# Kernel optimization log

Measured on AMD Instinct MI355X. Metric: run time of the kernel, lower is better.

Reference implementation:

```python
import jax, jax.numpy as jnp
import numpy as np

DIM, D_INNER, D_STATE, DT_RANK, D_CONV = 1024, 2048, 16, 64, 4
BATCH, SEQ = 2, 1024

def setup_inputs() -> dict:
    key = jax.random.key(0)
    ks = jax.random.split(key, 9)
    s = 0.02
    A = jnp.tile(jnp.arange(1, D_STATE + 1, dtype=jnp.float32), (D_INNER, 1))
    return {
        "x": jax.random.normal(ks[0], (BATCH, SEQ, DIM), jnp.float32),
        "in_proj_w": jax.random.normal(ks[1], (DIM, 2 * D_INNER), jnp.float32) * s,
        "conv_w": jax.random.normal(ks[2], (D_INNER, 1, D_CONV), jnp.float32) * 0.2,
        "conv_b": jax.random.normal(ks[3], (D_INNER,), jnp.float32) * 0.1,
        "x_proj_w": jax.random.normal(ks[4], (D_INNER, DT_RANK + 2 * D_STATE), jnp.float32) * s,
        "dt_proj_w": jax.random.normal(ks[5], (DT_RANK, D_INNER), jnp.float32) * s,
        "dt_proj_b": jax.random.normal(ks[6], (D_INNER,), jnp.float32) * 0.1,
        "A_log": jnp.log(A),
        "D_param": jnp.ones((D_INNER,), jnp.float32),
        "out_proj_w": jax.random.normal(ks[7], (D_INNER, DIM), jnp.float32) * s,
    }

def _silu(v):
    return v * jax.nn.sigmoid(v)

def _ssm_forward(x, in_proj_w, conv_w, conv_b, x_proj_w, dt_proj_w, dt_proj_b, A_log, D_param, out_proj_w):
    b, l, _ = x.shape
    d_inner, d_conv = conv_w.shape[0], conv_w.shape[2]
    dt_rank, n = dt_proj_w.shape[0], A_log.shape[1]
    # input projection and split into conv branch / gate branch
    x_and_res = x @ in_proj_w                      # (b, l, 2*d_inner)
    xp, res = x_and_res[..., :d_inner], x_and_res[..., d_inner:]
    # causal depthwise conv (torch pads d_conv-1 both sides then slices [:l])
    h = jax.lax.conv_general_dilated(
        xp.transpose(0, 2, 1), conv_w,
        window_strides=(1,), padding=[(d_conv - 1, 0)],
        dimension_numbers=("NCH", "OIH", "NCH"),
        feature_group_count=d_inner,
    ) + conv_b[None, :, None]                      # (b, d_inner, l)
    h = _silu(h.transpose(0, 2, 1))                # (b, l, d_inner)
    # input-dependent SSM parameters
    A = -jnp.exp(A_log)                            # (d_inner, n)
    x_dbl = h @ x_proj_w                           # (b, l, dt_rank + 2n)
    dlt, Bm, Cm = (x_dbl[..., :dt_rank],
                   x_dbl[..., dt_rank:dt_rank + n],
                   x_dbl[..., dt_rank + n:])
    delta = jax.nn.softplus(dlt @ dt_proj_w + dt_proj_b)   # (b, l, d_inner)
    # discretization
    deltaA = jnp.exp(jnp.einsum("bld,dn->bldn", delta, A))             # (b,l,d,n)
    deltaB_u = (delta * h)[..., None] * Bm[:, :, None, :]              # (b,l,d,n)
    # sequential selective scan over time via lax.scan
    def step(state, t):
        dA_t, dBu_t, c_t = t
        state = dA_t * state + dBu_t               # (b, d, n)
        y_t = jnp.einsum("bdn,bn->bd", state, c_t)
        return state, y_t
    init = jnp.zeros((b, d_inner, n), h.dtype)
    _, ys = jax.lax.scan(step, init,
                         (deltaA.transpose(1, 0, 2, 3),
                          deltaB_u.transpose(1, 0, 2, 3),
                          Cm.transpose(1, 0, 2)))
    y = ys.transpose(1, 0, 2) + h * D_param        # (b, l, d_inner)
    y = y * _silu(res)
    return y @ out_proj_w                          # (b, l, dim)

def reference(x, in_proj_w, conv_w, conv_b, x_proj_w, dt_proj_w, dt_proj_b, A_log, D_param, out_proj_w):
    return _ssm_forward(x, in_proj_w, conv_w, conv_b, x_proj_w, dt_proj_w, dt_proj_b, A_log, D_param, out_proj_w)
```

## Files before the change

### kernel.cpp

```cpp
#include <hip/hip_runtime.h>
#include <hip/hip_bf16.h>

#define DIM     1024
#define DINNER  2048
#define NSTATE  16
#define DTRANK  64
#define DCONV   4
#define BATCH   2
#define SEQ     1024
#define BL      (BATCH*SEQ)
#define XDBLW   96
#define NCHUNK  32
#define TCHUNK  32
#define KSLICE  16
#define G4SK    4
#define LOG2E   1.44269504088896f
#define LN2     0.69314718055995f

typedef __attribute__((ext_vector_type(4))) float  f32x4;
typedef __attribute__((ext_vector_type(8))) short  bf16x8;
typedef unsigned short ushort_t;

__device__ __forceinline__ ushort_t f2bf(float f) {
    union { float f; unsigned int u; } v; v.f = f;
    unsigned int lsb = (v.u >> 16) & 1u;
    v.u += 0x7fffu + lsb;
    return (ushort_t)(v.u >> 16);
}
__device__ __forceinline__ float bf2f(ushort_t h) {
    union { unsigned u; float f; } v; v.u = ((unsigned)h) << 16; return v.f;
}
__device__ __forceinline__ float hexp2(float x) { return __builtin_amdgcn_exp2f(x); }
__device__ __forceinline__ float hlog2(float x) { return __builtin_amdgcn_logf(x); }
__device__ __forceinline__ float hrcp(float x)  { return __builtin_amdgcn_rcpf(x); }
__device__ __forceinline__ float softplus_fast(float x) {
    float e = hexp2(-fabsf(x) * LOG2E);
    return fmaxf(x, 0.f) + LN2 * hlog2(1.f + e);
}
__device__ __forceinline__ float sigmoid_fast(float x) {
    return hrcp(1.f + hexp2(-x * LOG2E));
}

typedef __attribute__((address_space(1))) unsigned int gu32_t;
typedef __attribute__((address_space(3))) unsigned int lu32_t;
__device__ __forceinline__ void gload_lds16(const ushort_t* g, ushort_t* l) {
    __builtin_amdgcn_global_load_lds((const gu32_t*)(const void*)g,
                                     (lu32_t*)(void*)l, 16, 0, 0);
}

__global__ __launch_bounds__(256) void prep_fused(
    const float* __restrict__ Win,  ushort_t* __restrict__ WtIn,
    const float* __restrict__ Wout, ushort_t* __restrict__ WtOut,
    const float* __restrict__ Wxp,  ushort_t* __restrict__ WtXp,
    const float* __restrict__ x,    ushort_t* __restrict__ xb)
{
    __shared__ float tile[32][33];
    const int tid = threadIdx.x;
    const int tx = tid & 31, ty = tid >> 5;
    const int bid = blockIdx.x;

    const float* src; ushort_t* dst; int R, C, bx, by;
    if (bid < 4096)      { src = Win;  dst = WtIn;  R = 1024; C = 4096; int j = bid;        bx = j % 128; by = j / 128; }
    else if (bid < 6144) { src = Wout; dst = WtOut; R = 2048; C = 1024; int j = bid - 4096; bx = j % 32;  by = j / 32; }
    else if (bid < 6336) { src = Wxp;  dst = WtXp;  R = 2048; C = 96;   int j = bid - 6144; bx = j % 3;   by = j / 3; }
    else {
        int i = ((bid - 6336) * 256 + tid) * 4;
        f32x4 v = *(const f32x4*)(x + i);
        ushort_t r0 = f2bf(v[0]), r1 = f2bf(v[1]), r2 = f2bf(v[2]), r3 = f2bf(v[3]);
        *(uint2*)(xb + i) = make_uint2((unsigned)r0 | ((unsigned)r1 << 16),
                                       (unsigned)r2 | ((unsigned)r3 << 16));
        return;
    }

    const int r0 = by * 32, c0 = bx * 32;
    #pragma unroll
    for (int i = 0; i < 4; ++i)
        tile[ty + i * 8][tx] = src[(size_t)(r0 + ty + i * 8) * C + c0 + tx];
    __syncthreads();
    #pragma unroll
    for (int i = 0; i < 4; ++i)
        dst[(size_t)(c0 + ty + i * 8) * R + r0 + tx] = f2bf(tile[tx][ty + i * 8]);
}

__global__ __launch_bounds__(256) void gemm_lds(
    const ushort_t* __restrict__ A,  int lda,
    const ushort_t* __restrict__ Bt, int ldb,
    int K,
    float* __restrict__ Cf, ushort_t* __restrict__ Cb, int ldc)
{
    __shared__ ushort_t As[2][128 * 64];
    __shared__ ushort_t Bs[2][128 * 64];

    const int tid  = threadIdx.x;
    const int m0   = blockIdx.y * 128;
    const int n0   = blockIdx.x * 128;
    const int wid  = tid >> 6;
    const int lane = tid & 63;
    const int wm   = (wid >> 1) * 64;
    const int wn   = (wid & 1) * 64;
    const int lr   = lane & 15;

    int rq[4], gq[4], lo[4];
    #pragma unroll
    for (int q = 0; q < 4; ++q) {
        int c = q * 256 + tid;
        rq[q] = c >> 3;
        gq[q] = ((c & 7) ^ (rq[q] & 7)) * 8;
        lo[q] = (q * 256 + wid * 64) * 8;
    }

    f32x4 acc[4][4];
    #pragma unroll
    for (int m = 0; m < 4; ++m)
        #pragma unroll
        for (int n = 0; n < 4; ++n)
            acc[m][n] = (f32x4){0.f, 0.f, 0.f, 0.f};

    const int nk = K >> 6;

    #pragma unroll
    for (int q = 0; q < 4; ++q) {
        gload_lds16(A  + (size_t)(m0 + rq[q]) * lda + gq[q], &As[0][lo[q]]);
        gload_lds16(Bt + (size_t)(n0 + rq[q]) * ldb + gq[q], &Bs[0][lo[q]]);
    }

    for (int k = 0; k < nk; ++k) {
        const int cur = k & 1;
        if (k + 1 < nk) {
            const int k0 = (k + 1) << 6;
            #pragma unroll
            for (int q = 0; q < 4; ++q) {
                gload_lds16(A  + (size_t)(m0 + rq[q]) * lda + k0 + gq[q], &As[cur ^ 1][lo[q]]);
                gload_lds16(Bt + (size_t)(n0 + rq[q]) * ldb + k0 + gq[q], &Bs[cur ^ 1][lo[q]]);
            }
            asm volatile("s_waitcnt vmcnt(8)" ::: "memory");
        } else {
            asm volatile("s_waitcnt vmcnt(0)" ::: "memory");
        }
        __builtin_amdgcn_sched_barrier(0);
        __builtin_amdgcn_s_barrier();

        #pragma unroll
        for (int kk = 0; kk < 2; ++kk) {
            const int lg = (lane >> 4) + kk * 4;
            const int pc = (lg ^ (lr & 7)) * 8;
            bf16x8 af[4], bfr[4];
            #pragma unroll
            for (int m = 0; m < 4; ++m)
                af[m] = *(const bf16x8*)(&As[cur][(wm + m * 16 + lr) * 64 + pc]);
            #pragma unroll
            for (int n = 0; n < 4; ++n)
                bfr[n] = *(const bf16x8*)(&Bs[cur][(wn + n * 16 + lr) * 64 + pc]);
            #pragma unroll
            for (int m = 0; m < 4; ++m)
                #pragma unroll
                for (int n = 0; n < 4; ++n)
                    acc[m][n] = __builtin_amdgcn_mfma_f32_16x16x32_bf16(af[m], bfr[n], acc[m][n], 0, 0, 0);
        }
        __builtin_amdgcn_s_barrier();
    }

    const int rbase = (lane >> 4) * 4;
    #pragma unroll
    for (int m = 0; m < 4; ++m) {
        #pragma unroll
        for (int n = 0; n < 4; ++n) {
            int col = n0 + wn + n * 16 + lr;
            #pragma unroll
            for (int r = 0; r < 4; ++r) {
                int row = m0 + wm + m * 16 + rbase + r;
                float v = acc[m][n][r];
                if (Cf) Cf[(size_t)row * ldc + col] = v;
                if (Cb) Cb[(size_t)row * ldc + col] = f2bf(v);
            }
        }
    }
}

__global__ __launch_bounds__(256) void gemm_lds_sk(
    const ushort_t* __restrict__ A,  int lda,
    const ushort_t* __restrict__ Bt, int ldb,
    int klen,
    float* __restrict__ Part, int ldc, int mn)
{
    __shared__ ushort_t As[2][128 * 64];
    __shared__ ushort_t Bs[2][128 * 64];

    const int tid  = threadIdx.x;
    const int m0   = blockIdx.y * 128;
    const int n0   = blockIdx.x * 128;
    const int kb   = blockIdx.z * klen;
    float* Cf = Part + (size_t)blockIdx.z * mn;

    const int wid  = tid >> 6;
    const int lane = tid & 63;
    const int wm   = (wid >> 1) * 64;
    const int wn   = (wid & 1) * 64;
    const int lr   = lane & 15;

    int rq[4], gq[4], lo[4];
    #pragma unroll
    for (int q = 0; q < 4; ++q) {
        int c = q * 256 + tid;
        rq[q] = c >> 3;
        gq[q] = ((c & 7) ^ (rq[q] & 7)) * 8;
        lo[q] = (q * 256 + wid * 64) * 8;
    }

    f32x4 acc[4][4];
    #pragma unroll
    for (int m = 0; m < 4; ++m)
        #pragma unroll
        for (int n = 0; n < 4; ++n)
            acc[m][n] = (f32x4){0.f, 0.f, 0.f, 0.f};

    const int nk = klen >> 6;

    #pragma unroll
    for (int q = 0; q < 4; ++q) {
        gload_lds16(A  + (size_t)(m0 + rq[q]) * lda + kb + gq[q], &As[0][lo[q]]);
        gload_lds16(Bt + (size_t)(n0 + rq[q]) * ldb + kb + gq[q], &Bs[0][lo[q]]);
    }

    for (int k = 0; k < nk; ++k) {
        const int cur = k & 1;
        if (k + 1 < nk) {
            const int k0 = kb + ((k + 1) << 6);
            #pragma unroll
            for (int q = 0; q < 4; ++q) {
                gload_lds16(A  + (size_t)(m0 + rq[q]) * lda + k0 + gq[q], &As[cur ^ 1][lo[q]]);
                gload_lds16(Bt + (size_t)(n0 + rq[q]) * ldb + k0 + gq[q], &Bs[cur ^ 1][lo[q]]);
            }
            asm volatile("s_waitcnt vmcnt(8)" ::: "memory");
        } else {
            asm volatile("s_waitcnt vmcnt(0)" ::: "memory");
        }
        __builtin_amdgcn_sched_barrier(0);
        __builtin_amdgcn_s_barrier();

        #pragma unroll
        for (int kk = 0; kk < 2; ++kk) {
            const int lg = (lane >> 4) + kk * 4;
            const int pc = (lg ^ (lr & 7)) * 8;
            bf16x8 af[4], bfr[4];
            #pragma unroll
            for (int m = 0; m < 4; ++m)
                af[m] = *(const bf16x8*)(&As[cur][(wm + m * 16 + lr) * 64 + pc]);
            #pragma unroll
            for (int n = 0; n < 4; ++n)
                bfr[n] = *(const bf16x8*)(&Bs[cur][(wn + n * 16 + lr) * 64 + pc]);
            #pragma unroll
            for (int m = 0; m < 4; ++m)
                #pragma unroll
                for (int n = 0; n < 4; ++n)
                    acc[m][n] = __builtin_amdgcn_mfma_f32_16x16x32_bf16(af[m], bfr[n], acc[m][n], 0, 0, 0);
        }
        __builtin_amdgcn_s_barrier();
    }

    const int rbase = (lane >> 4) * 4;
    #pragma unroll
    for (int m = 0; m < 4; ++m) {
        #pragma unroll
        for (int n = 0; n < 4; ++n) {
            int col = n0 + wn + n * 16 + lr;
            #pragma unroll
            for (int r = 0; r < 4; ++r) {
                int row = m0 + wm + m * 16 + rbase + r;
                Cf[(size_t)row * ldc + col] = acc[m][n][r];
            }
        }
    }
}

__global__ __launch_bounds__(256) void g4_reduce(
    const float* __restrict__ Part, float* __restrict__ out)
{
    int i = (blockIdx.x * 256 + threadIdx.x) * 4;
    const size_t mn = (size_t)BL * DIM;
    f32x4 s = *(const f32x4*)(Part + i);
    #pragma unroll
    for (int z = 1; z < G4SK; ++z)
        s += *(const f32x4*)(Part + z * mn + i);
    *(f32x4*)(out + i) = s;
}

__global__ __launch_bounds__(256) void gemm_n96_splitk(
    const ushort_t* __restrict__ A,
    const ushort_t* __restrict__ Bt,
    float* __restrict__ Ppart)
{
    __shared__ ushort_t As[128 * 40];
    __shared__ ushort_t Bs[96 * 40];

    const int tid   = threadIdx.x;
    const int ks    = blockIdx.x;
    const int m0    = blockIdx.y * 128;
    const int kbase = ks * (DINNER / KSLICE);
    const int wid   = tid >> 6;
    const int lane  = tid & 63;
    const int wm    = wid * 32;
    const int lr    = lane & 15;
    const int lk    = (lane >> 4) * 8;

    f32x4 acc[2][6];
    #pragma unroll
    for (int m = 0; m < 2; ++m)
        #pragma unroll
        for (int n = 0; n < 6; ++n)
            acc[m][n] = (f32x4){0.f, 0.f, 0.f, 0.f};

    for (int k0 = kbase; k0 < kbase + DINNER / KSLICE; k0 += 32) {
        #pragma unroll
        for (int c = 0; c < 2; ++c) {
            int cid = tid + c * 256;
            int row = cid >> 2, ck = (cid & 3) * 8;
            *(uint4*)(&As[row * 40 + ck]) =
                *(const uint4*)(A + (size_t)(m0 + row) * DINNER + k0 + ck);
        }
        {
            int row = tid >> 2, ck = (tid & 3) * 8;
            *(uint4*)(&Bs[row * 40 + ck]) =
                *(const uint4*)(Bt + (size_t)row * DINNER + k0 + ck);
            if (tid < 128) {
                int cid = 256 + tid;
                int row2 = cid >> 2, ck2 = (cid & 3) * 8;
                *(uint4*)(&Bs[row2 * 40 + ck2]) =
                    *(const uint4*)(Bt + (size_t)row2 * DINNER + k0 + ck2);
            }
        }
        __syncthreads();

        bf16x8 af[2], bfr[6];
        #pragma unroll
        for (int m = 0; m < 2; ++m)
            af[m] = *(const bf16x8*)(&As[(wm + m * 16 + lr) * 40 + lk]);
        #pragma unroll
        for (int n = 0; n < 6; ++n)
            bfr[n] = *(const bf16x8*)(&Bs[(n * 16 + lr) * 40 + lk]);

        #pragma unroll
        for (int m = 0; m < 2; ++m)
            #pragma unroll
            for (int n = 0; n < 6; ++n)
                acc[m][n] = __builtin_amdgcn_mfma_f32_16x16x32_bf16(af[m], bfr[n], acc[m][n], 0, 0, 0);
        __syncthreads();
    }

    const int rbase = (lane >> 4) * 4;
    #pragma unroll
    for (int m = 0; m < 2; ++m) {
        #pragma unroll
        for (int n = 0; n < 6; ++n) {
            int col = n * 16 + lr;
            #pragma unroll
            for (int r = 0; r < 4; ++r) {
                int row = m0 + wm + m * 16 + rbase + r;
                Ppart[((size_t)ks * BL + row) * XDBLW + col] = acc[m][n][r];
            }
        }
    }
}

__global__ __launch_bounds__(256) void g2_reduce(
    const float* __restrict__ Ppart, float* __restrict__ xdbl)
{
    int idx = blockIdx.x * 256 + threadIdx.x;
    int row = idx / 24, cg = (idx % 24) * 4;
    f32x4 s = (f32x4){0.f, 0.f, 0.f, 0.f};
    #pragma unroll
    for (int ks = 0; ks < KSLICE; ++ks)
        s += *(const f32x4*)(Ppart + ((size_t)ks * BL + row) * XDBLW + cg);
    *(f32x4*)(xdbl + (size_t)row * XDBLW + cg) = s;
}

__global__ __launch_bounds__(256, 4) void delta_v6(
    const float* __restrict__ xdbl,
    const float* __restrict__ Wdt,
    const float* __restrict__ dtb,
    ushort_t* __restrict__ delta_bf)
{
    __shared__ float WS[64][256];
    __shared__ float dS[32][64];
    const int tid  = threadIdx.x;
    const int d0   = (blockIdx.x & 7) * 256;
    const int row0 = (blockIdx.x >> 3) * 32;

    #pragma unroll
    for (int i = 0; i < 16; ++i) {
        int c = i * 256 + tid;
        int k = c >> 6, co = (c & 63) * 4;
        *(f32x4*)&WS[k][co] = *(const f32x4*)(Wdt + (size_t)k * DINNER + d0 + co);
    }
    #pragma unroll
    for (int i = 0; i < 2; ++i) {
        int c = i * 256 + tid;
        int r = c >> 4, co = (c & 15) * 4;
        *(f32x4*)&dS[r][co] = *(const f32x4*)(xdbl + (size_t)(row0 + r) * XDBLW + co);
    }
    __syncthreads();

    const int w    = tid >> 6;
    const int lane = tid & 63;
    const int dd   = lane * 4;

    f32x4 acc[8];
    {
        f32x4 bb = *(const f32x4*)(dtb + d0 + dd);
        #pragma unroll
        for (int r = 0; r < 8; ++r) acc[r] = bb;
    }

    for (int kq = 0; kq < 16; ++kq) {
        f32x4 dv[8];
        #pragma unroll
        for (int r = 0; r < 8; ++r)
            dv[r] = *(const f32x4*)&dS[w * 8 + r][kq * 4];
        #pragma unroll
        for (int kk = 0; kk < 4; ++kk) {
            f32x4 wv = *(const f32x4*)&WS[kq * 4 + kk][dd];
            #pragma unroll
            for (int r = 0; r < 8; ++r) {
                float dk = dv[r][kk];
                acc[r][0] = fmaf(dk, wv[0], acc[r][0]);
                acc[r][1] = fmaf(dk, wv[1], acc[r][1]);
                acc[r][2] = fmaf(dk, wv[2], acc[r][2]);
                acc[r][3] = fmaf(dk, wv[3], acc[r][3]);
            }
        }
    }

    #pragma unroll
    for (int r = 0; r < 8; ++r) {
        const size_t rowb = (size_t)(row0 + w * 8 + r) * DINNER + d0;
        f32x4 v = acc[r];
        ushort_t o[4];
        #pragma unroll
        for (int j = 0; j < 4; ++j)
            o[j] = f2bf(softplus_fast(v[j]));
        *(uint2*)(delta_bf + rowb + dd) = make_uint2(
            (unsigned)o[0] | ((unsigned)o[1] << 16), (unsigned)o[2] | ((unsigned)o[3] << 16));
    }
}

__global__ __launch_bounds__(256) void conv_silu(
    const ushort_t* __restrict__ xrb,
    const float* __restrict__ convw,
    const float* __restrict__ convb,
    ushort_t* __restrict__ hb)
{
    const int d  = blockIdx.x * 256 + threadIdx.x;
    const int bt = blockIdx.y;
    const int t  = bt & (SEQ - 1);

    float acc = convb[d];
    #pragma unroll
    for (int j = 0; j < DCONV; ++j) {
        int tt = t + j - (DCONV - 1);
        if (tt >= 0)
            acc += convw[d * DCONV + j] * bf2f(xrb[(size_t)(bt + j - (DCONV - 1)) * 4096 + d]);
    }
    float h = acc * sigmoid_fast(acc);
    hb[(size_t)bt * DINNER + d] = f2bf(h);
}

__global__ __launch_bounds__(256) void scan_p1(
    const ushort_t* __restrict__ delta_bf,
    const ushort_t* __restrict__ hb,
    const float* __restrict__ xdbl,
    const float* __restrict__ Alog,
    float* __restrict__ Pbuf,
    float* __restrict__ Sbuf)
{
    const int d  = (blockIdx.x & 7) * 256 + threadIdx.x;
    const int bc = blockIdx.x >> 3;
    const int b  = bc >> 5;
    const int c  = bc & (NCHUNK - 1);
    const int t0 = c * TCHUNK;

    float A[NSTATE];
    #pragma unroll
    for (int q = 0; q < 4; ++q) {
        f32x4 al = *(const f32x4*)(Alog + (size_t)d * NSTATE + q * 4);
        #pragma unroll
        for (int j = 0; j < 4; ++j)
            A[q * 4 + j] = -hexp2(al[j] * LOG2E) * LOG2E;
    }

    float s[NSTATE], pp[NSTATE];
    #pragma unroll
    for (int n = 0; n < NSTATE; ++n) { s[n] = 0.f; pp[n] = 1.f; }

    for (int tt = 0; tt < TCHUNK; ++tt) {
        const size_t row = (size_t)(b * SEQ + t0 + tt);
        float dl = bf2f(delta_bf[row * DINNER + d]);
        float hv = bf2f(hb[row * DINNER + d]);
        float dlh = dl * hv;
        float Bv[NSTATE];
        #pragma unroll
        for (int q = 0; q < 4; ++q) {
            f32x4 bv = *(const f32x4*)(xdbl + row * XDBLW + DTRANK + q * 4);
            #pragma unroll
            for (int j = 0; j < 4; ++j) Bv[q * 4 + j] = bv[j];
        }
        #pragma unroll
        for (int n = 0; n < NSTATE; ++n) {
            float a = hexp2(dl * A[n]);
            s[n]  = fmaf(a, s[n], dlh * Bv[n]);
            pp[n] *= a;
        }
    }

    const size_t o = (((size_t)b * NCHUNK + c) * DINNER + d) * NSTATE;
    #pragma unroll
    for (int q = 0; q < 4; ++q) {
        *(f32x4*)(Sbuf + o + q * 4) = (f32x4){s[q*4+0], s[q*4+1], s[q*4+2], s[q*4+3]};
        *(f32x4*)(Pbuf + o + q * 4) = (f32x4){pp[q*4+0], pp[q*4+1], pp[q*4+2], pp[q*4+3]};
    }
}

__global__ __launch_bounds__(256) void scan_p2(
    const float* __restrict__ Pbuf, float* __restrict__ Sbuf)
{
    const int tid = blockIdx.x * 256 + threadIdx.x;
    const int n = tid & 15;
    const int d = (tid >> 4) & (DINNER - 1);
    const int b = tid >> 15;
    const size_t stride = (size_t)DINNER * NSTATE;
    size_t idx = ((size_t)b * NCHUNK * DINNER + d) * NSTATE + n;
    float cin = 0.f;
    for (int c = 0; c < NCHUNK; ++c, idx += stride) {
        float S = Sbuf[idx];
        float P = Pbuf[idx];
        Sbuf[idx] = cin;
        cin = fmaf(P, cin, S);
    }
}

__global__ __launch_bounds__(256) void scan_p3(
    const ushort_t* __restrict__ delta_bf,
    const ushort_t* __restrict__ hb,
    const float* __restrict__ xdbl,
    const ushort_t* __restrict__ xrb,
    const float* __restrict__ Alog,
    const float* __restrict__ Dp,
    const float* __restrict__ Sbuf,
    ushort_t* __restrict__ yb)
{
    const int d  = (blockIdx.x & 7) * 256 + threadIdx.x;
    const int bc = blockIdx.x >> 3;
    const int b  = bc >> 5;
    const int c  = bc & (NCHUNK - 1);
    const int t0 = c * TCHUNK;

    float A[NSTATE];
    #pragma unroll
    for (int q = 0; q < 4; ++q) {
        f32x4 al = *(const f32x4*)(Alog + (size_t)d * NSTATE + q * 4);
        #pragma unroll
        for (int j = 0; j < 4; ++j)
            A[q * 4 + j] = -hexp2(al[j] * LOG2E) * LOG2E;
    }
    const float Dd = Dp[d];

    float s[NSTATE];
    const size_t o = (((size_t)b * NCHUNK + c) * DINNER + d) * NSTATE;
    #pragma unroll
    for (int q = 0; q < 4; ++q) {
        f32x4 sv = *(const f32x4*)(Sbuf + o + q * 4);
        #pragma unroll
        for (int j = 0; j < 4; ++j) s[q * 4 + j] = sv[j];
    }

    for (int tt = 0; tt < TCHUNK; ++tt) {
        const size_t row = (size_t)(b * SEQ + t0 + tt);
        float dl = bf2f(delta_bf[row * DINNER + d]);
        float hv = bf2f(hb[row * DINNER + d]);
        float rv = bf2f(xrb[row * 4096 + DINNER + d]);
        float dlh = dl * hv;
        float Bv[NSTATE], Cv[NSTATE];
        #pragma unroll
        for (int q = 0; q < 4; ++q) {
            f32x4 bv = *(const f32x4*)(xdbl + row * XDBLW + DTRANK + q * 4);
            f32x4 cv = *(const f32x4*)(xdbl + row * XDBLW + DTRANK + NSTATE + q * 4);
            #pragma unroll
            for (int j = 0; j < 4; ++j) { Bv[q*4+j] = bv[j]; Cv[q*4+j] = cv[j]; }
        }
        float y = 0.f;
        #pragma unroll
        for (int n = 0; n < NSTATE; ++n) {
            float a = hexp2(dl * A[n]);
            s[n] = fmaf(a, s[n], dlh * Bv[n]);
            y = fmaf(s[n], Cv[n], y);
        }
        y = fmaf(hv, Dd, y);
        y = y * rv * sigmoid_fast(rv);
        yb[row * DINNER + d] = f2bf(y);
    }
}

extern "C" void kernel_launch(void* const* d_in, const int* in_sizes, int n_in,
                              void* d_out, int out_size, void* d_ws, size_t ws_size,
                              hipStream_t stream)
{
    const float* x     = (const float*)d_in[0];
    const float* Win   = (const float*)d_in[1];
    const float* convw = (const float*)d_in[2];
    const float* convb = (const float*)d_in[3];
    const float* Wxp   = (const float*)d_in[4];
    const float* Wdt   = (const float*)d_in[5];
    const float* dtb   = (const float*)d_in[6];
    const float* Alog  = (const float*)d_in[7];
    const float* Dp    = (const float*)d_in[8];
    const float* Wout  = (const float*)d_in[9];
    float* out = (float*)d_out;

    char* base = (char*)d_ws; size_t off = 0;
    auto alloc = [&](size_t bytes) -> char* {
        char* q = base + off;
        off = (off + bytes + 255) & ~(size_t)255;
        return q;
    };
    ushort_t* WtIn   = (ushort_t*)alloc((size_t)4096 * 1024 * 2);
    ushort_t* WtOut  = (ushort_t*)alloc((size_t)1024 * 2048 * 2);
    ushort_t* WtXp   = (ushort_t*)alloc((size_t)96   * 2048 * 2);
    ushort_t* xb     = (ushort_t*)alloc((size_t)BL * DIM * 2);
    ushort_t* xrb    = (ushort_t*)alloc((size_t)BL * 4096 * 2);
    ushort_t* hb     = (ushort_t*)alloc((size_t)BL * DINNER * 2);
    float*    xdbl   = (float*)   alloc((size_t)BL * XDBLW * 4);
    ushort_t* dltbf  = (ushort_t*)alloc((size_t)BL * DINNER * 2);
    ushort_t* yb     = (ushort_t*)alloc((size_t)BL * DINNER * 2);
    float*    Pbuf   = (float*)   alloc((size_t)BATCH * NCHUNK * DINNER * NSTATE * 4);
    float*    Sbuf   = (float*)   alloc((size_t)BATCH * NCHUNK * DINNER * NSTATE * 4);
    float*    Ppart  = (float*)   alloc((size_t)KSLICE * BL * XDBLW * 4);
    float*    G4part = (float*)   alloc((size_t)G4SK * BL * DIM * 4);
    (void)ws_size;

    prep_fused<<<dim3(8384), 256, 0, stream>>>(Win, WtIn, Wout, WtOut, Wxp, WtXp, x, xb);

    gemm_lds<<<dim3(4096/128, BL/128), 256, 0, stream>>>(
        xb, DIM, WtIn, DIM, DIM, nullptr, xrb, 2*DINNER);

    conv_silu<<<dim3(DINNER/256, BL), 256, 0, stream>>>(xrb, convw, convb, hb);

    gemm_n96_splitk<<<dim3(KSLICE, BL/128), 256, 0, stream>>>(hb, WtXp, Ppart);
    g2_reduce<<<dim3(BL * 24 / 256), 256, 0, stream>>>(Ppart, xdbl);

    delta_v6<<<dim3(8 * (BL / 32)), 256, 0, stream>>>(xdbl, Wdt, dtb, dltbf);

    scan_p1<<<dim3(8 * BATCH * NCHUNK), 256, 0, stream>>>(dltbf, hb, xdbl, Alog, Pbuf, Sbuf);
    scan_p2<<<dim3(BATCH * DINNER * NSTATE / 256), 256, 0, stream>>>(Pbuf, Sbuf);
    scan_p3<<<dim3(8 * BATCH * NCHUNK), 256, 0, stream>>>(dltbf, hb, xdbl, xrb, Alog, Dp, Sbuf, yb);

    gemm_lds_sk<<<dim3(DIM/128, BL/128, G4SK), 256, 0, stream>>>(
        yb, DINNER, WtOut, DINNER, DINNER/G4SK, G4part, DIM, BL*DIM);
    g4_reduce<<<dim3(BL*DIM/4/256), 256, 0, stream>>>(G4part, out);
}
```

Baseline: 147.7 us.

## Remap GEMM tiles per XCD, vectorize conv_silu, batch loads in scan_p2

GEMM block indices are remapped so that consecutive blocks dispatched to the same XCD work on neighbouring N tiles, which should improve L2 reuse of weights. conv_silu now has each thread handle 8 channels, using 16-byte bf16x8 loads and stores instead of scalar accesses, with one block per time step. scan_p2 issues all 32 chunk loads up front into registers before the serial recurrence, so memory latency overlaps instead of accumulating across iterations. The costs are higher register use and remap logic that assumes gridDim.x is a multiple of 8.

```diff
diff --git a/kernel.cpp b/kernel.cpp
--- a/kernel.cpp
+++ b/kernel.cpp
@@ -48,6 +48,14 @@
                                      (lu32_t*)(void*)l, 16, 0, 0);
 }
 
+__device__ __forceinline__ void xcd_remap(int lin, int gx, int gy, int& mi, int& ni) {
+    const int c = lin & 7;
+    const int o = lin >> 3;
+    const int ncs = gx >> 3;
+    ni = c * ncs + o / gy;
+    mi = o % gy;
+}
+
 __global__ __launch_bounds__(256) void prep_fused(
     const float* __restrict__ Win,  ushort_t* __restrict__ WtIn,
     const float* __restrict__ Wout, ushort_t* __restrict__ WtOut,
@@ -92,8 +100,10 @@
     __shared__ ushort_t Bs[2][128 * 64];
 
     const int tid  = threadIdx.x;
-    const int m0   = blockIdx.y * 128;
-    const int n0   = blockIdx.x * 128;
+    int mi, ni;
+    xcd_remap(blockIdx.y * gridDim.x + blockIdx.x, gridDim.x, gridDim.y, mi, ni);
+    const int m0 = mi * 128;
+    const int n0 = ni * 128;
     const int wid  = tid >> 6;
     const int lane = tid & 63;
     const int wm   = (wid >> 1) * 64;
@@ -187,8 +197,10 @@
     __shared__ ushort_t Bs[2][128 * 64];
 
     const int tid  = threadIdx.x;
-    const int m0   = blockIdx.y * 128;
-    const int n0   = blockIdx.x * 128;
+    int mi, ni;
+    xcd_remap(blockIdx.y * gridDim.x + blockIdx.x, gridDim.x, gridDim.y, mi, ni);
+    const int m0 = mi * 128;
+    const int n0 = ni * 128;
     const int kb   = blockIdx.z * klen;
     float* Cf = Part + (size_t)blockIdx.z * mn;
 
@@ -449,19 +461,36 @@
     const float* __restrict__ convb,
     ushort_t* __restrict__ hb)
 {
-    const int d  = blockIdx.x * 256 + threadIdx.x;
-    const int bt = blockIdx.y;
+    const int bt = blockIdx.x;
     const int t  = bt & (SEQ - 1);
-
-    float acc = convb[d];
+    const int d0 = threadIdx.x * 8;
+
+    bf16x8 xv[DCONV];
     #pragma unroll
     for (int j = 0; j < DCONV; ++j) {
         int tt = t + j - (DCONV - 1);
         if (tt >= 0)
-            acc += convw[d * DCONV + j] * bf2f(xrb[(size_t)(bt + j - (DCONV - 1)) * 4096 + d]);
-    }
-    float h = acc * sigmoid_fast(acc);
-    hb[(size_t)bt * DINNER + d] = f2bf(h);
+            xv[j] = *(const bf16x8*)(xrb + (size_t)(bt + j - (DCONV - 1)) * 4096 + d0);
+        else
+            xv[j] = (bf16x8){0,0,0,0,0,0,0,0};
+    }
+
+    ushort_t o[8];
+    #pragma unroll
+    for (int dd = 0; dd < 8; ++dd) {
+        f32x4 w = *(const f32x4*)(convw + (size_t)(d0 + dd) * DCONV);
+        float acc = convb[d0 + dd];
+        #pragma unroll
+        for (int j = 0; j < DCONV; ++j)
+            acc = fmaf(w[j], bf2f((ushort_t)xv[j][dd]), acc);
+        o[dd] = f2bf(acc * sigmoid_fast(acc));
+    }
+    uint4 pk;
+    pk.x = (unsigned)o[0] | ((unsigned)o[1] << 16);
+    pk.y = (unsigned)o[2] | ((unsigned)o[3] << 16);
+    pk.z = (unsigned)o[4] | ((unsigned)o[5] << 16);
+    pk.w = (unsigned)o[6] | ((unsigned)o[7] << 16);
+    *(uint4*)(hb + (size_t)bt * DINNER + d0) = pk;
 }
 
 __global__ __launch_bounds__(256) void scan_p1(
@@ -527,14 +556,24 @@
     const int d = (tid >> 4) & (DINNER - 1);
     const int b = tid >> 15;
     const size_t stride = (size_t)DINNER * NSTATE;
-    size_t idx = ((size_t)b * NCHUNK * DINNER + d) * NSTATE + n;
+    const size_t base = ((size_t)b * NCHUNK * DINNER + d) * NSTATE + n;
+
+    float S[NCHUNK], P[NCHUNK];
+    #pragma unroll
+    for (int c = 0; c < NCHUNK; ++c) {
+        S[c] = Sbuf[base + c * stride];
+        P[c] = Pbuf[base + c * stride];
+    }
     float cin = 0.f;
-    for (int c = 0; c < NCHUNK; ++c, idx += stride) {
-        float S = Sbuf[idx];
-        float P = Pbuf[idx];
-        Sbuf[idx] = cin;
-        cin = fmaf(P, cin, S);
-    }
+    float O[NCHUNK];
+    #pragma unroll
+    for (int c = 0; c < NCHUNK; ++c) {
+        O[c] = cin;
+        cin = fmaf(P[c], cin, S[c]);
+    }
+    #pragma unroll
+    for (int c = 0; c < NCHUNK; ++c)
+        Sbuf[base + c * stride] = O[c];
 }
 
 __global__ __launch_bounds__(256) void scan_p3(
@@ -641,7 +680,7 @@
     gemm_lds<<<dim3(4096/128, BL/128), 256, 0, stream>>>(
         xb, DIM, WtIn, DIM, DIM, nullptr, xrb, 2*DINNER);
 
-    conv_silu<<<dim3(DINNER/256, BL), 256, 0, stream>>>(xrb, convw, convb, hb);
+    conv_silu<<<dim3(BL), 256, 0, stream>>>(xrb, convw, convb, hb);
 
     gemm_n96_splitk<<<dim3(KSLICE, BL/128), 256, 0, stream>>>(hb, WtXp, Ppart);
     g2_reduce<<<dim3(BL * 24 / 256), 256, 0, stream>>>(Ppart, xdbl);
```

Result: faster. 140.8 us (-4.7%).
